# Kernel tuning notes

Hardware: AMD Instinct MI355X
Metric: run time of the kernel (lower is better)

The kernel has to match this reference:

```python
import jax, jax.numpy as jnp
import numpy as np

D = 512
H = 4
DK = D // H
N_ACTOR = 4096
N_BV = 4096
NEG = jnp.float32(-1e9)  # stands in for -inf; exp underflows to exactly 0 in fp32


def setup_inputs() -> dict:
    key = jax.random.key(0)
    k1, k2, k3, k4, k5, k6, k7, k8 = jax.random.split(key, 8)
    a_z = jax.random.normal(k1, (N_ACTOR, D), dtype=jnp.float32)
    bv_z = jax.random.normal(k2, (N_BV, D), dtype=jnp.float32)
    mask = jax.random.uniform(k3, (N_ACTOR, N_BV)) > 0.5
    weight = jax.random.normal(k4, (N_ACTOR, N_BV), dtype=jnp.float32)
    # nn.MultiheadAttention parameters (packed in_proj, out_proj)
    in_proj_w = jax.random.normal(k5, (3 * D, D), dtype=jnp.float32) * 0.02
    in_proj_b = jax.random.normal(k6, (3 * D,), dtype=jnp.float32) * 0.02
    out_w = jax.random.normal(k7, (D, D), dtype=jnp.float32) * 0.02
    out_b = jax.random.normal(k8, (D,), dtype=jnp.float32) * 0.02
    return {"a_z": a_z, "bv_z": bv_z, "mask": mask, "weight": weight,
            "in_proj_w": in_proj_w, "in_proj_b": in_proj_b,
            "out_w": out_w, "out_b": out_b}


def reference(a_z, bv_z, mask, weight, in_proj_w, in_proj_b, out_w, out_b):
    n, d = a_z.shape
    m = bv_z.shape[0]
    a = jnp.nan_to_num(a_z, nan=0.0, posinf=1.0, neginf=-1.0)
    kv = jnp.nan_to_num(bv_z, nan=0.0, posinf=1.0, neginf=-1.0)
    w = jnp.nan_to_num(weight, nan=0.0, posinf=1.0, neginf=-1.0)
    mf = mask.astype(a.dtype)
    valid = jnp.any(mask, axis=1)  # actors with at least one unmasked key

    # attn_mask = weight masked with -inf at padded keys (covers key_padding_mask too)
    bias = jnp.where(mask, w, NEG)  # [n, m]

    wq, wk, wv = jnp.split(in_proj_w, 3, axis=0)
    bq, bk, bv = jnp.split(in_proj_b, 3, axis=0)
    q = ((a @ wq.T + bq).reshape(n, H, DK)) * (1.0 / np.sqrt(DK))
    k = (kv @ wk.T + bk).reshape(m, H, DK)
    v = (kv @ wv.T + bv).reshape(m, H, DK)

    scores = jnp.einsum('nhd,mhd->nhm', q, k) + bias[:, None, :]
    attn = jax.nn.softmax(scores, axis=-1)                  # [n, h, m]
    ctx = jnp.einsum('nhm,mhd->nhd', attn, v).reshape(n, d)
    out = ctx @ out_w.T + out_b                              # out_proj

    # topic alignment: mean over head-chunks of the projected output
    topic = out.reshape(n, H, DK).mean(axis=1)               # [n, dk]

    # influence: softmax-normalized weight scores dotted with avg attn weights
    aw = attn.mean(axis=1) * mf                              # head-averaged attn, masked
    norm_scores = jax.nn.softmax(bias, axis=-1) * mf
    influence = jnp.sum(norm_scores * aw, axis=-1)           # [n]

    # actors with no valid key are scattered back as zeros
    topic = jnp.where(valid[:, None], topic, 0.0)
    influence = jnp.where(valid, influence, 0.0)
    return topic, influence
```

## Files before the change

kernel.cpp:

```cpp
#include <hip/hip_runtime.h>
#include <hip/hip_bf16.h>
#include <cstdint>
#include <cstddef>


typedef __attribute__((ext_vector_type(8))) short bf16x8;
typedef __attribute__((ext_vector_type(4))) short bf16x4;
typedef __attribute__((ext_vector_type(4))) float f32x4;

#define MFMA32(a, b, c) __builtin_amdgcn_mfma_f32_16x16x32_bf16((a), (b), (c), 0, 0, 0)
#define MFMA16(a, b, c) __builtin_amdgcn_mfma_f32_16x16x16bf16_1k((a), (b), (c), 0, 0, 0)

static __device__ __forceinline__ short f2b(float x) {
  union { float f; unsigned u; } v; v.f = x;
  unsigned r = v.u + 0x7fffu + ((v.u >> 16) & 1u);
  return (short)(r >> 16);
}

__global__ __launch_bounds__(256) void k_qkv(
    const float* __restrict__ a, const float* __restrict__ kv,
    const float* __restrict__ w, const float* __restrict__ bias,
    short* __restrict__ Qb, short* __restrict__ Kp, short* __restrict__ Vp)
{
  __shared__ short As[128 * 40];
  __shared__ short Bs[64 * 40];
  const int blk = blockIdx.x;
  const int bm = blk % 32, bn = blk / 32;
  const int m0 = bm * 128, n0 = bn * 64;
  const float* __restrict__ Ain = (bn < 8) ? a : kv;
  const int tid = threadIdx.x;
  const int lane = tid & 63, wvi = tid >> 6;
  const int wm = (wvi >> 1) * 64, wn = (wvi & 1) * 32;
  const int c = lane & 15, g = lane >> 4;
  const int srA = tid >> 1, scA = (tid & 1) * 16;
  const int srB = tid >> 2, scB = (tid & 3) * 8;

  f32x4 acc[4][2];
#pragma unroll
  for (int i = 0; i < 4; ++i)
#pragma unroll
    for (int j = 0; j < 2; ++j) acc[i][j] = (f32x4)0.f;

  for (int k0 = 0; k0 < 512; k0 += 32) {
    const float* ap = Ain + (size_t)(m0 + srA) * 512 + k0 + scA;
#pragma unroll
    for (int j = 0; j < 4; ++j) {
      f32x4 av = *(const f32x4*)(ap + 4 * j);
      bf16x4 as;
      as.x = f2b(av.x); as.y = f2b(av.y); as.z = f2b(av.z); as.w = f2b(av.w);
      *(bf16x4*)(&As[srA * 40 + scA + 4 * j]) = as;
    }
    const float* bp = w + (size_t)(n0 + srB) * 512 + k0 + scB;
#pragma unroll
    for (int j = 0; j < 2; ++j) {
      f32x4 bv = *(const f32x4*)(bp + 4 * j);
      bf16x4 bs;
      bs.x = f2b(bv.x); bs.y = f2b(bv.y); bs.z = f2b(bv.z); bs.w = f2b(bv.w);
      *(bf16x4*)(&Bs[srB * 40 + scB + 4 * j]) = bs;
    }
    __syncthreads();
    bf16x8 af[4], bfg[2];
#pragma unroll
    for (int t = 0; t < 4; ++t)
      af[t] = *(const bf16x8*)(&As[(wm + t * 16 + c) * 40 + g * 8]);
#pragma unroll
    for (int t = 0; t < 2; ++t)
      bfg[t] = *(const bf16x8*)(&Bs[(wn + t * 16 + c) * 40 + g * 8]);
#pragma unroll
    for (int rt = 0; rt < 4; ++rt)
#pragma unroll
      for (int ct = 0; ct < 2; ++ct)
        acc[rt][ct] = MFMA32(af[rt], bfg[ct], acc[rt][ct]);
    __syncthreads();
  }

#pragma unroll
  for (int ct = 0; ct < 2; ++ct) {
    const int col = n0 + wn + ct * 16 + c;
    const float bj = bias[col];
#pragma unroll
    for (int rt = 0; rt < 4; ++rt) {
      const int row = m0 + wm + rt * 16 + g * 4;
      const int mc = row >> 4;
      if (col < 512) {
#pragma unroll
        for (int r = 0; r < 4; ++r)
          Qb[(size_t)(row + r) * 512 + col] = f2b((acc[rt][ct][r] + bj) * 0.08838834764831843f);
      } else if (col < 1024) {
        const int colK = col - 512;
        const int h = colK >> 7, dk = colK & 127;
        const int ks = dk >> 5, gk = (dk >> 3) & 3, j = dk & 7;
        short* base = Kp + (size_t)((((h * 256 + mc) * 4 + ks) * 64) + gk * 16 + g * 4) * 8 + j;
#pragma unroll
        for (int r = 0; r < 4; ++r) base[r * 8] = f2b(acc[rt][ct][r] + bj);
      } else {
        const int colV = col - 1024;
        const int h = colV >> 7, db = (colV & 127) >> 4, cv = colV & 15;
        bf16x4 pk;
#pragma unroll
        for (int r = 0; r < 4; ++r) pk[r] = f2b(acc[rt][ct][r] + bj);
        *(bf16x4*)(Vp + (size_t)((((h * 256 + mc) * 8 + db) * 64) + g * 16 + cv) * 4) = pk;
      }
    }
  }
}

__global__ __launch_bounds__(256, 4) void k_attn(
    const short* __restrict__ Qb, const short* __restrict__ Kp,
    const short* __restrict__ Vp, const float* __restrict__ wgt,
    const int* __restrict__ msk, const int S,
    short* __restrict__ Opart, float* __restrict__ lpart,
    float* __restrict__ cipart, float* __restrict__ lbpart)
{
  const int bx = blockIdx.x;
  const int sp = bx % S, rb = bx / S;
  const int n0 = rb * 16;
  const int mlen = 4096 / S;
  const int mc0 = (sp * mlen) >> 4;
  const int nch = mlen >> 4;
  const int tid = threadIdx.x;
  const int lane = tid & 63, h = tid >> 6;
  const int c = lane & 15, g = lane >> 4;

  bf16x8 qf[4];
#pragma unroll
  for (int ks = 0; ks < 4; ++ks)
    qf[ks] = *(const bf16x8*)(Qb + (size_t)(n0 + c) * 512 + h * 128 + ks * 32 + g * 8);

  f32x4 O[8];
#pragma unroll
  for (int db = 0; db < 8; ++db) O[db] = (f32x4)0.f;
  float lh = 0.f, lb = 0.f, ci = 0.f;

  const short* Kw = Kp + (size_t)h * 524288 + (size_t)lane * 8 + (size_t)mc0 * 2048;
  const short* Vw = Vp + (size_t)h * 524288 + (size_t)lane * 4 + (size_t)mc0 * 2048;
  const int* mbase_p = msk + (size_t)(n0 + c) * 4096 + g * 4 + (size_t)mc0 * 16;
  const float* wbase_p = wgt + (size_t)(n0 + c) * 4096 + g * 4 + (size_t)mc0 * 16;

  int4 mkN = *(const int4*)(mbase_p);
  f32x4 wvN = *(const f32x4*)(wbase_p);

  for (int t = 0; t < nch; ++t) {
    bf16x8 kf[4];
#pragma unroll
    for (int ks = 0; ks < 4; ++ks)
      kf[ks] = *(const bf16x8*)(Kw + t * 2048 + ks * 512);
    bf16x4 vf[8];
#pragma unroll
    for (int db = 0; db < 8; ++db)
      vf[db] = *(const bf16x4*)(Vw + t * 2048 + db * 256);

    const int4 mkC = mkN;
    const f32x4 wvC = wvN;
    const int tn = (t + 1 < nch) ? (t + 1) : t;
    mkN = *(const int4*)(mbase_p + tn * 16);
    wvN = *(const f32x4*)(wbase_p + tn * 16);

    f32x4 Sv = (f32x4)0.f;
#pragma unroll
    for (int ks = 0; ks < 4; ++ks) Sv = MFMA32(kf[ks], qf[ks], Sv);
    const float e0 = mkC.x ? __expf(wvC.x) : 0.f;
    const float e1 = mkC.y ? __expf(wvC.y) : 0.f;
    const float e2 = mkC.z ? __expf(wvC.z) : 0.f;
    const float e3 = mkC.w ? __expf(wvC.w) : 0.f;
    const float p0 = __expf(Sv[0]) * e0, p1 = __expf(Sv[1]) * e1;
    const float p2 = __expf(Sv[2]) * e2, p3 = __expf(Sv[3]) * e3;
    lh += (p0 + p1) + (p2 + p3);
    lb += (e0 + e1) + (e2 + e3);
    ci += (p0 * e0 + p1 * e1) + (p2 * e2 + p3 * e3);
    bf16x4 pa;
    pa[0] = f2b(p0); pa[1] = f2b(p1); pa[2] = f2b(p2); pa[3] = f2b(p3);
#pragma unroll
    for (int db = 0; db < 8; ++db)
      O[db] = MFMA16(pa, vf[db], O[db]);
  }

  lh += __shfl_xor(lh, 16, 64); lh += __shfl_xor(lh, 32, 64);
  lb += __shfl_xor(lb, 16, 64); lb += __shfl_xor(lb, 32, 64);
  ci += __shfl_xor(ci, 16, 64); ci += __shfl_xor(ci, 32, 64);

  float inv[4];
#pragma unroll
  for (int r = 0; r < 4; ++r)
    inv[r] = 1.f / fmaxf(__shfl(lh, 4 * g + r, 64), 1e-30f);
#pragma unroll
  for (int db = 0; db < 8; ++db)
#pragma unroll
    for (int r = 0; r < 4; ++r)
      Opart[(size_t)sp * (4096 * 512) + (size_t)(n0 + g * 4 + r) * 512 +
            h * 128 + db * 16 + c] = f2b(O[db][r] * inv[r]);

  if (g == 0) {
    const int row = n0 + c;
    lpart[((size_t)sp * 4 + h) * 4096 + row] = lh;
    cipart[((size_t)sp * 4 + h) * 4096 + row] = ci;
    if (h == 0) lbpart[(size_t)sp * 4096 + row] = lb;
  }
}

__global__ __launch_bounds__(256) void k_comb(
    const short* __restrict__ Opart, const float* __restrict__ lpart,
    const float* __restrict__ cipart, const float* __restrict__ lbpart,
    const int S, short* __restrict__ ctxb, float* __restrict__ validw,
    float* __restrict__ infl)
{
  const int tid = threadIdx.x;
  const int rloc = tid >> 5, cseg = tid & 31;
  const int row = blockIdx.x * 8 + rloc;
  const int col0 = cseg * 16;
  const int h = col0 >> 7;

  float l[4], ciS[4], lb = 0.f;
#pragma unroll
  for (int hh = 0; hh < 4; ++hh) { l[hh] = 0.f; ciS[hh] = 0.f; }
  for (int s = 0; s < S; ++s) {
#pragma unroll
    for (int hh = 0; hh < 4; ++hh) {
      l[hh]   += lpart[((size_t)s * 4 + hh) * 4096 + row];
      ciS[hh] += cipart[((size_t)s * 4 + hh) * 4096 + row];
    }
    lb += lbpart[(size_t)s * 4096 + row];
  }

  float acc[16];
#pragma unroll
  for (int j = 0; j < 16; ++j) acc[j] = 0.f;
  const float linv = 1.f / fmaxf(l[h], 1e-30f);
  for (int s = 0; s < S; ++s) {
    const float w_s = lpart[((size_t)s * 4 + h) * 4096 + row] * linv;
    const bf16x8 o0 = *(const bf16x8*)(Opart + (size_t)s * (4096 * 512) + (size_t)row * 512 + col0);
    const bf16x8 o1 = *(const bf16x8*)(Opart + (size_t)s * (4096 * 512) + (size_t)row * 512 + col0 + 8);
#pragma unroll
    for (int j = 0; j < 8; ++j) {
      union { unsigned u; float f; } v0, v1;
      v0.u = ((unsigned)(unsigned short)o0[j]) << 16;
      v1.u = ((unsigned)(unsigned short)o1[j]) << 16;
      acc[j]     += w_s * v0.f;
      acc[8 + j] += w_s * v1.f;
    }
  }
  bf16x8 c0, c1;
#pragma unroll
  for (int j = 0; j < 8; ++j) { c0[j] = f2b(acc[j]); c1[j] = f2b(acc[8 + j]); }
  *(bf16x8*)(ctxb + (size_t)row * 512 + col0) = c0;
  *(bf16x8*)(ctxb + (size_t)row * 512 + col0 + 8) = c1;

  if (cseg == 0) {
    validw[row] = (lb > 0.f) ? 1.f : 0.f;
    float s_ = 0.f;
#pragma unroll
    for (int hh = 0; hh < 4; ++hh) s_ += ciS[hh] / fmaxf(l[hh], 1e-30f);
    infl[row] = (lb > 0.f) ? s_ / (4.f * lb) : 0.f;
  }
}

__global__ void k_fold(const float* __restrict__ ow, const float* __restrict__ ob,
                       short* __restrict__ Wf, float* __restrict__ bfo)
{
  const int idx = blockIdx.x * 256 + threadIdx.x;
  if (idx < 128 * 512) {
    const int dk = idx >> 9, d = idx & 511;
    const float s = 0.25f * (ow[(size_t)dk * 512 + d] + ow[(size_t)(dk + 128) * 512 + d] +
                             ow[(size_t)(dk + 256) * 512 + d] + ow[(size_t)(dk + 384) * 512 + d]);
    Wf[(size_t)dk * 512 + d] = f2b(s);
  }
  if (idx < 128) bfo[idx] = 0.25f * (ob[idx] + ob[idx + 128] + ob[idx + 256] + ob[idx + 384]);
}

__global__ __launch_bounds__(256) void k_out(
    const short* __restrict__ ctxb, const short* __restrict__ Wf,
    const float* __restrict__ bfo, const float* __restrict__ validw,
    float* __restrict__ topic)
{
  const int tid = threadIdx.x;
  const int lane = tid & 63, wvi = tid >> 6;
  const int m0 = blockIdx.x * 16;
  const int c = lane & 15, g = lane >> 4;

  f32x4 acc[2];
  acc[0] = (f32x4)0.f; acc[1] = (f32x4)0.f;

  for (int k0 = 0; k0 < 512; k0 += 32) {
    const bf16x8 af = *(const bf16x8*)(ctxb + (size_t)(m0 + c) * 512 + k0 + g * 8);
#pragma unroll
    for (int dbl = 0; dbl < 2; ++dbl) {
      const bf16x8 bfr = *(const bf16x8*)(Wf + (size_t)(wvi * 32 + dbl * 16 + c) * 512 + k0 + g * 8);
      acc[dbl] = MFMA32(af, bfr, acc[dbl]);
    }
  }

#pragma unroll
  for (int r = 0; r < 4; ++r) {
    const int row = m0 + g * 4 + r;
    const float va = validw[row];
#pragma unroll
    for (int dbl = 0; dbl < 2; ++dbl) {
      const int col = wvi * 32 + dbl * 16 + c;
      const float vl = (va > 0.5f) ? (acc[dbl][r] + bfo[col]) : 0.f;
      topic[(size_t)row * 128 + col] = vl;
    }
  }
}

extern "C" void kernel_launch(void* const* d_in, const int* in_sizes, int n_in,
                              void* d_out, int out_size, void* d_ws, size_t ws_size,
                              hipStream_t stream) {
  const float* a_z  = (const float*)d_in[0];
  const float* bv_z = (const float*)d_in[1];
  const int*   mask = (const int*)d_in[2];
  const float* wgt  = (const float*)d_in[3];
  const float* ipw  = (const float*)d_in[4];
  const float* ipb  = (const float*)d_in[5];
  const float* ow   = (const float*)d_in[6];
  const float* ob   = (const float*)d_in[7];
  float* topic = (float*)d_out;
  float* infl  = (float*)d_out + 4096 * 128;

  const size_t MB = (size_t)1 << 20;
  char* ws = (char*)d_ws;
  short* Qb     = (short*)(ws);
  short* Kp     = (short*)(ws + 4 * MB);
  short* Vp     = (short*)(ws + 8 * MB);
  short* ctxb   = (short*)(ws + 12 * MB);
  float* validw = (float*)(ws + 16 * MB);
  short* Wf     = (short*)(ws + 16 * MB + (64 << 10));
  float* bfo    = (float*)(ws + 16 * MB + (224 << 10));
  const size_t pbase0 = 16 * MB + (256 << 10);

  auto need = [&](int S) { return pbase0 + (size_t)S * (4 * MB + (144 << 10)); };
  int S = 8;
  while (S > 1 && need(S) > ws_size) S >>= 1;

  char* pbase = ws + pbase0;
  short* Opart  = (short*)(pbase);
  float* lpart  = (float*)(pbase + (size_t)S * 4 * MB);
  float* cipart = (float*)(pbase + (size_t)S * 4 * MB + ((size_t)S << 16));
  float* lbpart = (float*)(pbase + (size_t)S * 4 * MB + ((size_t)S << 17));

  k_qkv <<<768, 256, 0, stream>>>(a_z, bv_z, ipw, ipb, Qb, Kp, Vp);
  k_fold<<<256, 256, 0, stream>>>(ow, ob, Wf, bfo);
  k_attn<<<256 * S, 256, 0, stream>>>(Qb, Kp, Vp, wgt, mask, S, Opart, lpart, cipart, lbpart);
  k_comb<<<512, 256, 0, stream>>>(Opart, lpart, cipart, lbpart, S, ctxb, validw, infl);
  k_out <<<256, 256, 0, stream>>>(ctxb, Wf, bfo, validw, topic);
}
```

Baseline: 355.7 us.

## Add producer wave streaming mask and weight into LDS ring via async loads

The attention kernel gains a fifth wavefront that acts as a producer. It prefetches the mask and weight tiles several chunks ahead into an 8-slot LDS ring using global_load_lds, and the four compute waves read them from LDS after a per-chunk barrier. This replaces each compute wave's direct global loads of the mask and weights, which were prefetched only one chunk ahead, and is meant to hide their latency. In exchange it adds a block-wide barrier every chunk, uses more LDS and more threads per block, and relies on a fragile vmcnt-based synchronisation with a swizzled layout.

```diff
diff --git a/kernel.cpp b/kernel.cpp
--- a/kernel.cpp
+++ b/kernel.cpp
@@ -105,13 +105,21 @@
   }
 }
 
-__global__ __launch_bounds__(256, 4) void k_attn(
+#define MW_D    7
+#define MW_RING 8
+
+typedef const __attribute__((address_space(1))) void* gas_p;
+typedef __attribute__((address_space(3))) void* las_p;
+
+__global__ __launch_bounds__(320, 4) void k_attn(
     const short* __restrict__ Qb, const short* __restrict__ Kp,
     const short* __restrict__ Vp, const float* __restrict__ wgt,
     const int* __restrict__ msk, const int S,
     short* __restrict__ Opart, float* __restrict__ lpart,
     float* __restrict__ cipart, float* __restrict__ lbpart)
 {
+  __shared__ int mw_lds[MW_RING * 512];
+
   const int bx = blockIdx.x;
   const int sp = bx % S, rb = bx / S;
   const int n0 = rb * 16;
@@ -119,7 +127,36 @@
   const int mc0 = (sp * mlen) >> 4;
   const int nch = mlen >> 4;
   const int tid = threadIdx.x;
-  const int lane = tid & 63, h = tid >> 6;
+  const int lane = tid & 63, wvi = tid >> 6;
+
+  if (wvi == 4) {
+    const int r = lane >> 2;
+    const int qsw = ((lane & 3) + r) & 3;
+    const int* msrc = msk + (size_t)(n0 + r) * 4096 + qsw * 4 + (size_t)mc0 * 16;
+    const float* wsrc = wgt + (size_t)(n0 + r) * 4096 + qsw * 4 + (size_t)mc0 * 16;
+#pragma unroll
+    for (int d = 0; d < MW_D; ++d) {
+      const int slot = d & (MW_RING - 1);
+      __builtin_amdgcn_global_load_lds((gas_p)(msrc + (size_t)d * 16),
+                                       (las_p)(&mw_lds[slot * 512]), 16, 0, 0);
+      __builtin_amdgcn_global_load_lds((gas_p)(wsrc + (size_t)d * 16),
+                                       (las_p)(&mw_lds[slot * 512 + 256]), 16, 0, 0);
+    }
+    for (int t = 0; t < nch; ++t) {
+      asm volatile("s_waitcnt vmcnt(12)" ::: "memory");
+      __builtin_amdgcn_s_barrier();
+      const int tn = t + MW_D;
+      const int slot = tn & (MW_RING - 1);
+      const size_t tsrc = (size_t)((tn < nch) ? tn : (nch - 1));
+      __builtin_amdgcn_global_load_lds((gas_p)(msrc + tsrc * 16),
+                                       (las_p)(&mw_lds[slot * 512]), 16, 0, 0);
+      __builtin_amdgcn_global_load_lds((gas_p)(wsrc + tsrc * 16),
+                                       (las_p)(&mw_lds[slot * 512 + 256]), 16, 0, 0);
+    }
+    return;
+  }
+
+  const int h = wvi;
   const int c = lane & 15, g = lane >> 4;
 
   bf16x8 qf[4];
@@ -134,13 +171,12 @@
 
   const short* Kw = Kp + (size_t)h * 524288 + (size_t)lane * 8 + (size_t)mc0 * 2048;
   const short* Vw = Vp + (size_t)h * 524288 + (size_t)lane * 4 + (size_t)mc0 * 2048;
-  const int* mbase_p = msk + (size_t)(n0 + c) * 4096 + g * 4 + (size_t)mc0 * 16;
-  const float* wbase_p = wgt + (size_t)(n0 + c) * 4096 + g * 4 + (size_t)mc0 * 16;
-
-  int4 mkN = *(const int4*)(mbase_p);
-  f32x4 wvN = *(const f32x4*)(wbase_p);
+  const int msel = (4 * c + ((g - c) & 3)) * 4;
 
   for (int t = 0; t < nch; ++t) {
+    __builtin_amdgcn_s_barrier();
+    asm volatile("" ::: "memory");
+    const int slot = t & (MW_RING - 1);
     bf16x8 kf[4];
 #pragma unroll
     for (int ks = 0; ks < 4; ++ks)
@@ -149,12 +185,8 @@
 #pragma unroll
     for (int db = 0; db < 8; ++db)
       vf[db] = *(const bf16x4*)(Vw + t * 2048 + db * 256);
-
-    const int4 mkC = mkN;
-    const f32x4 wvC = wvN;
-    const int tn = (t + 1 < nch) ? (t + 1) : t;
-    mkN = *(const int4*)(mbase_p + tn * 16);
-    wvN = *(const f32x4*)(wbase_p + tn * 16);
+    const int4 mkC = *(const int4*)&mw_lds[slot * 512 + msel];
+    const f32x4 wvC = *(const f32x4*)((const float*)&mw_lds[slot * 512 + 256 + msel]);
 
     f32x4 Sv = (f32x4)0.f;
 #pragma unroll
@@ -339,7 +371,7 @@
 
   k_qkv <<<768, 256, 0, stream>>>(a_z, bv_z, ipw, ipb, Qb, Kp, Vp);
   k_fold<<<256, 256, 0, stream>>>(ow, ob, Wf, bfo);
-  k_attn<<<256 * S, 256, 0, stream>>>(Qb, Kp, Vp, wgt, mask, S, Opart, lpart, cipart, lbpart);
+  k_attn<<<256 * S, 320, 0, stream>>>(Qb, Kp, Vp, wgt, mask, S, Opart, lpart, cipart, lbpart);
   k_comb<<<512, 256, 0, stream>>>(Opart, lpart, cipart, lbpart, S, ctxb, validw, infl);
   k_out <<<256, 256, 0, stream>>>(ctxb, Wf, bfo, validw, topic);
 }
```

New measurement: 371.2 us. +4.4%, slower.

## Precompute masked exp(weight) into MFMA-fragment layout before attention

Applied to the files above, without the earlier changes.

Adds a pre-pass kernel that reads the mask and weight matrices once, computes exp(weight) where unmasked, and writes the result into a layout that matches the attention kernel's MFMA fragment order. The attention kernel then does one coalesced 16-byte load per chunk instead of strided mask and weight loads plus exp. It also splits the QK MFMA chain into two independent accumulators to shorten the dependency chain. The cost is an extra 64MB workspace buffer and an extra pass over the mask and weight data. The old path is kept as a fallback when the workspace is too small.

```diff
diff --git a/kernel.cpp b/kernel.cpp
--- a/kernel.cpp
+++ b/kernel.cpp
@@ -105,12 +105,40 @@
   }
 }
 
+__global__ __launch_bounds__(256) void k_pre(
+    const int* __restrict__ msk, const float* __restrict__ wgt,
+    float* __restrict__ Ep)
+{
+  const int b = blockIdx.x;
+  const int rb = b >> 3, ks8 = b & 7;
+  const int t = threadIdx.x;
+  const int c = t >> 4;
+  const int row = rb * 16 + c;
+  const int lt = t & 15;
+  const int g = t & 3;
+#pragma unroll
+  for (int p = 0; p < 8; ++p) {
+    const int k0 = ks8 * 512 + p * 64 + lt * 4;
+    const int4 mk = *(const int4*)(msk + (size_t)row * 4096 + k0);
+    const f32x4 wv = *(const f32x4*)(wgt + (size_t)row * 4096 + k0);
+    f32x4 ev;
+    ev[0] = mk.x ? __expf(wv.x) : 0.f;
+    ev[1] = mk.y ? __expf(wv.y) : 0.f;
+    ev[2] = mk.z ? __expf(wv.z) : 0.f;
+    ev[3] = mk.w ? __expf(wv.w) : 0.f;
+    const int mc = k0 >> 4;
+    *(f32x4*)(Ep + ((size_t)(rb * 256 + mc) * 64 + g * 16 + c) * 4) = ev;
+  }
+}
+
+template<int EP>
 __global__ __launch_bounds__(256, 4) void k_attn(
     const short* __restrict__ Qb, const short* __restrict__ Kp,
     const short* __restrict__ Vp, const float* __restrict__ wgt,
     const int* __restrict__ msk, const int S,
     short* __restrict__ Opart, float* __restrict__ lpart,
-    float* __restrict__ cipart, float* __restrict__ lbpart)
+    float* __restrict__ cipart, float* __restrict__ lbpart,
+    const float* __restrict__ Ep)
 {
   const int bx = blockIdx.x;
   const int sp = bx % S, rb = bx / S;
@@ -134,45 +162,78 @@
 
   const short* Kw = Kp + (size_t)h * 524288 + (size_t)lane * 8 + (size_t)mc0 * 2048;
   const short* Vw = Vp + (size_t)h * 524288 + (size_t)lane * 4 + (size_t)mc0 * 2048;
-  const int* mbase_p = msk + (size_t)(n0 + c) * 4096 + g * 4 + (size_t)mc0 * 16;
-  const float* wbase_p = wgt + (size_t)(n0 + c) * 4096 + g * 4 + (size_t)mc0 * 16;
-
-  int4 mkN = *(const int4*)(mbase_p);
-  f32x4 wvN = *(const f32x4*)(wbase_p);
-
-  for (int t = 0; t < nch; ++t) {
-    bf16x8 kf[4];
-#pragma unroll
-    for (int ks = 0; ks < 4; ++ks)
-      kf[ks] = *(const bf16x8*)(Kw + t * 2048 + ks * 512);
-    bf16x4 vf[8];
-#pragma unroll
-    for (int db = 0; db < 8; ++db)
-      vf[db] = *(const bf16x4*)(Vw + t * 2048 + db * 256);
-
-    const int4 mkC = mkN;
-    const f32x4 wvC = wvN;
-    const int tn = (t + 1 < nch) ? (t + 1) : t;
-    mkN = *(const int4*)(mbase_p + tn * 16);
-    wvN = *(const f32x4*)(wbase_p + tn * 16);
-
-    f32x4 Sv = (f32x4)0.f;
-#pragma unroll
-    for (int ks = 0; ks < 4; ++ks) Sv = MFMA32(kf[ks], qf[ks], Sv);
-    const float e0 = mkC.x ? __expf(wvC.x) : 0.f;
-    const float e1 = mkC.y ? __expf(wvC.y) : 0.f;
-    const float e2 = mkC.z ? __expf(wvC.z) : 0.f;
-    const float e3 = mkC.w ? __expf(wvC.w) : 0.f;
-    const float p0 = __expf(Sv[0]) * e0, p1 = __expf(Sv[1]) * e1;
-    const float p2 = __expf(Sv[2]) * e2, p3 = __expf(Sv[3]) * e3;
-    lh += (p0 + p1) + (p2 + p3);
-    lb += (e0 + e1) + (e2 + e3);
-    ci += (p0 * e0 + p1 * e1) + (p2 * e2 + p3 * e3);
-    bf16x4 pa;
-    pa[0] = f2b(p0); pa[1] = f2b(p1); pa[2] = f2b(p2); pa[3] = f2b(p3);
-#pragma unroll
-    for (int db = 0; db < 8; ++db)
-      O[db] = MFMA16(pa, vf[db], O[db]);
+
+  if (EP) {
+    const float* Eb = Ep + ((size_t)(rb * 256 + mc0) * 64 + lane) * 4;
+    f32x4 evC = *(const f32x4*)(Eb);
+    for (int t = 0; t < nch; ++t) {
+      bf16x8 kf[4];
+#pragma unroll
+      for (int ks = 0; ks < 4; ++ks)
+        kf[ks] = *(const bf16x8*)(Kw + t * 2048 + ks * 512);
+      bf16x4 vf[8];
+#pragma unroll
+      for (int db = 0; db < 8; ++db)
+        vf[db] = *(const bf16x4*)(Vw + t * 2048 + db * 256);
+      const f32x4 ev = evC;
+      const int tn = (t + 1 < nch) ? (t + 1) : t;
+      evC = *(const f32x4*)(Eb + (size_t)tn * 256);
+
+      f32x4 Sa = (f32x4)0.f, Sb = (f32x4)0.f;
+      Sa = MFMA32(kf[0], qf[0], Sa);
+      Sb = MFMA32(kf[2], qf[2], Sb);
+      Sa = MFMA32(kf[1], qf[1], Sa);
+      Sb = MFMA32(kf[3], qf[3], Sb);
+      const float p0 = __expf(Sa[0] + Sb[0]) * ev[0];
+      const float p1 = __expf(Sa[1] + Sb[1]) * ev[1];
+      const float p2 = __expf(Sa[2] + Sb[2]) * ev[2];
+      const float p3 = __expf(Sa[3] + Sb[3]) * ev[3];
+      lh += (p0 + p1) + (p2 + p3);
+      lb += (ev[0] + ev[1]) + (ev[2] + ev[3]);
+      ci += (p0 * ev[0] + p1 * ev[1]) + (p2 * ev[2] + p3 * ev[3]);
+      bf16x4 pa;
+      pa[0] = f2b(p0); pa[1] = f2b(p1); pa[2] = f2b(p2); pa[3] = f2b(p3);
+#pragma unroll
+      for (int db = 0; db < 8; ++db)
+        O[db] = MFMA16(pa, vf[db], O[db]);
+    }
+  } else {
+    const int* mbase_p = msk + (size_t)(n0 + c) * 4096 + g * 4 + (size_t)mc0 * 16;
+    const float* wbase_p = wgt + (size_t)(n0 + c) * 4096 + g * 4 + (size_t)mc0 * 16;
+    int4 mkN = *(const int4*)(mbase_p);
+    f32x4 wvN = *(const f32x4*)(wbase_p);
+    for (int t = 0; t < nch; ++t) {
+      bf16x8 kf[4];
+#pragma unroll
+      for (int ks = 0; ks < 4; ++ks)
+        kf[ks] = *(const bf16x8*)(Kw + t * 2048 + ks * 512);
+      bf16x4 vf[8];
+#pragma unroll
+      for (int db = 0; db < 8; ++db)
+        vf[db] = *(const bf16x4*)(Vw + t * 2048 + db * 256);
+      const int4 mkC = mkN;
+      const f32x4 wvC = wvN;
+      const int tn = (t + 1 < nch) ? (t + 1) : t;
+      mkN = *(const int4*)(mbase_p + tn * 16);
+      wvN = *(const f32x4*)(wbase_p + tn * 16);
+      f32x4 Sv = (f32x4)0.f;
+#pragma unroll
+      for (int ks = 0; ks < 4; ++ks) Sv = MFMA32(kf[ks], qf[ks], Sv);
+      const float e0 = mkC.x ? __expf(wvC.x) : 0.f;
+      const float e1 = mkC.y ? __expf(wvC.y) : 0.f;
+      const float e2 = mkC.z ? __expf(wvC.z) : 0.f;
+      const float e3 = mkC.w ? __expf(wvC.w) : 0.f;
+      const float p0 = __expf(Sv[0]) * e0, p1 = __expf(Sv[1]) * e1;
+      const float p2 = __expf(Sv[2]) * e2, p3 = __expf(Sv[3]) * e3;
+      lh += (p0 + p1) + (p2 + p3);
+      lb += (e0 + e1) + (e2 + e3);
+      ci += (p0 * e0 + p1 * e1) + (p2 * e2 + p3 * e3);
+      bf16x4 pa;
+      pa[0] = f2b(p0); pa[1] = f2b(p1); pa[2] = f2b(p2); pa[3] = f2b(p3);
+#pragma unroll
+      for (int db = 0; db < 8; ++db)
+        O[db] = MFMA16(pa, vf[db], O[db]);
+    }
   }
 
   lh += __shfl_xor(lh, 16, 64); lh += __shfl_xor(lh, 32, 64);
@@ -325,13 +386,20 @@
   float* validw = (float*)(ws + 16 * MB);
   short* Wf     = (short*)(ws + 16 * MB + (64 << 10));
   float* bfo    = (float*)(ws + 16 * MB + (224 << 10));
-  const size_t pbase0 = 16 * MB + (256 << 10);
-
-  auto need = [&](int S) { return pbase0 + (size_t)S * (4 * MB + (144 << 10)); };
-  int S = 8;
-  while (S > 1 && need(S) > ws_size) S >>= 1;
-
-  char* pbase = ws + pbase0;
+  const size_t fixed = 16 * MB + (256 << 10);
+  const size_t epBytes = (size_t)4096 * 4096 * 4;
+
+  auto need = [&](int S, int ep) {
+    return fixed + (ep ? epBytes : 0) + (size_t)S * (4 * MB + (144 << 10));
+  };
+  int S = 8, useEp = 1;
+  while (S > 1 && need(S, 1) > ws_size) S >>= 1;
+  if (need(S, 1) > ws_size) {
+    useEp = 0; S = 8;
+    while (S > 1 && need(S, 0) > ws_size) S >>= 1;
+  }
+  float* Ep = useEp ? (float*)(ws + fixed) : nullptr;
+  char* pbase = ws + fixed + (useEp ? epBytes : 0);
   short* Opart  = (short*)(pbase);
   float* lpart  = (float*)(pbase + (size_t)S * 4 * MB);
   float* cipart = (float*)(pbase + (size_t)S * 4 * MB + ((size_t)S << 16));
@@ -339,7 +407,14 @@
 
   k_qkv <<<768, 256, 0, stream>>>(a_z, bv_z, ipw, ipb, Qb, Kp, Vp);
   k_fold<<<256, 256, 0, stream>>>(ow, ob, Wf, bfo);
-  k_attn<<<256 * S, 256, 0, stream>>>(Qb, Kp, Vp, wgt, mask, S, Opart, lpart, cipart, lbpart);
+  if (useEp) {
+    k_pre<<<2048, 256, 0, stream>>>(mask, wgt, Ep);
+    k_attn<1><<<256 * S, 256, 0, stream>>>(Qb, Kp, Vp, wgt, mask, S,
+                                           Opart, lpart, cipart, lbpart, Ep);
+  } else {
+    k_attn<0><<<256 * S, 256, 0, stream>>>(Qb, Kp, Vp, wgt, mask, S,
+                                           Opart, lpart, cipart, lbpart, Ep);
+  }
   k_comb<<<512, 256, 0, stream>>>(Opart, lpart, cipart, lbpart, S, ctxb, validw, infl);
   k_out <<<256, 256, 0, stream>>>(ctxb, Wf, bfo, validw, topic);
 }
```

Measured after the change: 330.4 us. 7.1% less time.
